# Kernel optimization log

Measured on AMD Instinct MI355X. Metric: run time of the kernel, lower is better.

Reference implementation:

```python
import jax, jax.numpy as jnp
import numpy as np

N, C, L, E, H = 2000, 4, 5000, 64000, 512
REP = 207  # length after conv front-end: floor((floor((5000-11)/4)+1 - 11)/6)+1


def setup_inputs() -> dict:
    key = jax.random.key(0)
    ks = jax.random.split(key, 10)

    def init(k, shape, fan_in):
        return jax.random.normal(k, shape, jnp.float32) / np.sqrt(fan_in).astype(np.float32)

    x = jax.random.normal(ks[0], (N, C, L), jnp.float32)
    edge_index = jax.random.randint(ks[1], (2, E), 0, N)
    return dict(
        x=x, edge_index=edge_index,
        w1=init(ks[2], (16, C, 1), C), b1=jnp.zeros(16, jnp.float32),
        w2=init(ks[3], (4, 4, 11), 4 * 11), b2=jnp.zeros(4, jnp.float32),
        w3=init(ks[4], (1, 4, 11), 4 * 11), b3=jnp.zeros(1, jnp.float32),
        gcn_w=init(ks[5], (REP, H), REP), gcn_b=jnp.zeros(H, jnp.float32),
        lin_w=init(ks[6], (REP, H), REP), lin_b=jnp.zeros(H, jnp.float32),
        gate_w=init(ks[7], (H, H), H), gate_b=jnp.zeros(H, jnp.float32),
        bn_gamma=jnp.ones(H, jnp.float32), bn_beta=jnp.zeros(H, jnp.float32),
    )


def _conv1d(x, w, b, stride):
    # x: [N, Cin, L], w: [Cout, Cin, K] (torch OIH layout), VALID padding
    y = jax.lax.conv_general_dilated(x, w, (stride,), 'VALID',
                                     dimension_numbers=('NCH', 'OIH', 'NCH'))
    return y + b[None, :, None]


def _gcn_conv(feat, edge_index, w, b, n):
    # GCNConv: x@W, add self-loops, sym-normalize, scatter-add, + bias
    h = feat @ w                                      # [N, H]
    loops = jnp.arange(n)
    src = jnp.concatenate([edge_index[0], loops])
    dst = jnp.concatenate([edge_index[1], loops])
    deg = jax.ops.segment_sum(jnp.ones_like(src, h.dtype), dst, num_segments=n)
    dinv = jax.lax.rsqrt(deg)                         # deg >= 1 due to self-loops
    norm = dinv[src] * dinv[dst]                      # [E+N]
    out = jax.ops.segment_sum(h[src] * norm[:, None], dst, num_segments=n)
    return out + b


def reference(x, edge_index, w1, b1, w2, b2, w3, b3,
              gcn_w, gcn_b, lin_w, lin_b, gate_w, gate_b, bn_gamma, bn_beta):
    n = x.shape[0]
    # conv front-end (dropout layers are identity at inference)
    h = jax.nn.relu(_conv1d(x, w1, b1, 1))            # [N, 16, L]
    # MaxPool1d(k=4,s=4) applied on permuted [N, L, 16] == pool over channel dim
    h = h.reshape(n, 4, 4, L).max(axis=2)             # [N, 4, L]
    h = jax.nn.relu(_conv1d(h, w2, b2, 4))            # [N, 4, 1248]
    h = jax.nn.relu(_conv1d(h, w3, b3, 6))            # [N, 1, 207]
    feat = h[:, 0, :]                                 # squeeze -> [N, REP]
    # GCN + gated fusion
    z = jnp.tanh(_gcn_conv(feat, edge_index, gcn_w, gcn_b, n))
    g = jax.nn.sigmoid(z @ gate_w + gate_b)
    xl = feat @ lin_w + lin_b
    out = jax.nn.relu((1.0 - g) * xl + g * z)
    # BatchNorm over node dim (batch statistics, training-mode semantics)
    mean = out.mean(axis=0)
    var = out.var(axis=0)
    out = (out - mean) * jax.lax.rsqrt(var + 1e-5) * bn_gamma + bn_beta
    return out
```

## Files before the change

### kernel.cpp

```cpp
#include <hip/hip_runtime.h>
#include <hip/hip_bf16.h>
#include <cstddef>

#define NN 2000
#define CC 4
#define LL1 5000
#define LL2 1248
#define LL3 207
#define FSTR 208
#define HH 512
#define EE 64000

__device__ float g_feat[NN * FSTR];
__device__ float g_aggf[NN * FSTR];
__device__ float g_z[NN * HH];
__device__ float g_xl[NN * HH];
__device__ float g_obuf[NN * HH];
__device__ float g_dinv[NN];
__device__ float g_colsum[HH];
__device__ float g_colsq[HH];
__device__ int   g_cnt[NN];
__device__ int   g_cursor[NN];
__device__ int   g_off[NN];
__device__ int   g_bucket[EE];

#define MCH 1256
__global__ __launch_bounds__(256) void conv_chain(
    const float* __restrict__ x, const int* __restrict__ ei, const int E,
    const float* __restrict__ w1, const float* __restrict__ b1,
    const float* __restrict__ w2, const float* __restrict__ b2,
    const float* __restrict__ w3, const float* __restrict__ b3)
{
    __shared__ __align__(16) float sm[4 * MCH];
    __shared__ __align__(16) float sy[4 * LL2];

    const int tid = threadIdx.x;
    const int node = blockIdx.x;

    if (node < 2) {
        int i = node * 256 + tid;
        g_colsum[i] = 0.f; g_colsq[i] = 0.f;
    }
    if (node < 250) {
        for (int e = node * 256 + tid; e < E; e += 250 * 256)
            atomicAdd(&g_cnt[ei[E + e]], 1);
    }

    const float* xb = x + (size_t)node * (CC * LL1);

    float w1r[64], b1r[16];
#pragma unroll
    for (int i = 0; i < 64; ++i) w1r[i] = w1[i];
#pragma unroll
    for (int i = 0; i < 16; ++i) b1r[i] = b1[i];

    float4 xA[2][4], xB[2][4];

    auto issueL = [&](int cc, float4 (&dst)[2][4]) {
#pragma unroll
        for (int it = 0; it < 2; ++it) {
            const int g4 = tid + it * 256;
            if (g4 < 314) {
                const int l = 1248 * cc + 4 * g4;
#pragma unroll
                for (int ch = 0; ch < 4; ++ch)
                    dst[it][ch] = *(const float4*)(xb + ch * LL1 + l);
            }
        }
    };

    auto stage1 = [&](float4 (&src)[2][4]) {
#pragma unroll
        for (int it = 0; it < 2; ++it) {
            const int g4 = tid + it * 256;
            if (g4 < 314) {
                float xs[4][4];
#pragma unroll
                for (int ch = 0; ch < 4; ++ch)
                    *(float4*)xs[ch] = src[it][ch];
#pragma unroll
                for (int g = 0; g < 4; ++g) {
                    float mv[4];
#pragma unroll
                    for (int li = 0; li < 4; ++li) {
                        float best = -1e30f;
#pragma unroll
                        for (int j = 0; j < 4; ++j) {
                            int o = g * 4 + j;
                            float v = b1r[o] + w1r[o*4+0]*xs[0][li] + w1r[o*4+1]*xs[1][li]
                                             + w1r[o*4+2]*xs[2][li] + w1r[o*4+3]*xs[3][li];
                            best = fmaxf(best, v);
                        }
                        mv[li] = fmaxf(best, 0.f);
                    }
                    *(float4*)&sm[g * MCH + 4 * g4] = make_float4(mv[0], mv[1], mv[2], mv[3]);
                }
            }
        }
    };

    auto stage2 = [&](int cc) {
        const int T0 = 312 * cc;
#pragma unroll 1
        for (int pair = 0; pair < 2; ++pair) {
            const float* wp = w2 + 88 * pair;
            float wo[88];
#pragma unroll
            for (int i = 0; i < 88; ++i) wo[i] = wp[i];
            const float bo0 = b2[2 * pair], bo1 = b2[2 * pair + 1];
            for (int T = tid; T < 312; T += 256) {
                float a0 = bo0, a1 = bo1;
#pragma unroll
                for (int i = 0; i < 4; ++i) {
                    const float* mp = sm + i * MCH + 4 * T;
                    float4 u0 = *(const float4*)mp;
                    float4 u1 = *(const float4*)(mp + 4);
                    float4 u2 = *(const float4*)(mp + 8);
                    float v[12] = {u0.x, u0.y, u0.z, u0.w,
                                   u1.x, u1.y, u1.z, u1.w,
                                   u2.x, u2.y, u2.z, u2.w};
#pragma unroll
                    for (int k = 0; k < 11; ++k) {
                        a0 += wo[i * 11 + k] * v[k];
                        a1 += wo[44 + i * 11 + k] * v[k];
                    }
                }
                sy[(2 * pair) * LL2 + T0 + T]     = fmaxf(a0, 0.f);
                sy[(2 * pair + 1) * LL2 + T0 + T] = fmaxf(a1, 0.f);
            }
        }
    };

    issueL(0, xA);
    issueL(1, xB);
    stage1(xA); __syncthreads(); stage2(0); __syncthreads();
    issueL(2, xA);
    stage1(xB); __syncthreads(); stage2(1); __syncthreads();
    issueL(3, xB);
    stage1(xA); __syncthreads(); stage2(2); __syncthreads();
    stage1(xB); __syncthreads(); stage2(3); __syncthreads();

    if (tid < FSTR) {
        float acc = 0.f;
        if (tid < LL3) {
            acc = b3[0];
#pragma unroll
            for (int i = 0; i < 4; ++i)
#pragma unroll
                for (int k = 0; k < 11; ++k)
                    acc += w3[i * 11 + k] * sy[i * LL2 + 6 * tid + k];
            acc = fmaxf(acc, 0.f);
        }
        g_feat[(size_t)node * FSTR + tid] = acc;
    }
}

__global__ __launch_bounds__(256) void scan_dinv() {
    const int tid = threadIdx.x;
    const int base = tid * 8;
    int c[8];
#pragma unroll
    for (int k = 0; k < 8; ++k) c[k] = (base + k < NN) ? g_cnt[base + k] : 0;
    int pre[8]; int s = 0;
#pragma unroll
    for (int k = 0; k < 8; ++k) { pre[k] = s; s += c[k]; }
    const int lane = tid & 63;
    int ws = s;
#pragma unroll
    for (int d = 1; d < 64; d <<= 1) {
        int t = __shfl_up(ws, d, 64);
        if (lane >= d) ws += t;
    }
    __shared__ int wsum[4];
    const int wid = tid >> 6;
    if (lane == 63) wsum[wid] = ws;
    __syncthreads();
    int woff = 0;
#pragma unroll
    for (int w = 0; w < 4; ++w) if (w < wid) woff += wsum[w];
    const int toff = woff + ws - s;
#pragma unroll
    for (int k = 0; k < 8; ++k) {
        const int i = base + k;
        if (i < NN) {
            g_off[i] = toff + pre[k];
            g_dinv[i] = rsqrtf(1.0f + (float)c[k]);
        }
    }
}

__global__ void bucket_fill(const int* __restrict__ ei, int E) {
    int e = blockIdx.x * 256 + threadIdx.x;
    if (e < E) {
        int d = ei[E + e];
        int p = atomicAdd(&g_cursor[d], 1);
        g_bucket[g_off[d] + p] = ei[e];
    }
}

__global__ __launch_bounds__(256) void agg_feat() {
    const int sub = threadIdx.x >> 6;
    const int lane = threadIdx.x & 63;
    const int d = blockIdx.x * 4 + sub;
    if (lane >= 52) return;
    const float di = g_dinv[d];
    const int nb = g_cnt[d];
    const int base = g_off[d];
    const size_t co = (size_t)lane * 4;
    float4 a = *(const float4*)(g_feat + (size_t)d * FSTR + co);
    float ax = a.x * di, ay = a.y * di, az = a.z * di, aw = a.w * di;
    int j = 0;
    for (; j + 1 < nb; j += 2) {
        int s0 = g_bucket[base + j];
        int s1 = g_bucket[base + j + 1];
        float w0 = g_dinv[s0], w1 = g_dinv[s1];
        float4 f0 = *(const float4*)(g_feat + (size_t)s0 * FSTR + co);
        float4 f1 = *(const float4*)(g_feat + (size_t)s1 * FSTR + co);
        ax += f0.x * w0 + f1.x * w1;
        ay += f0.y * w0 + f1.y * w1;
        az += f0.z * w0 + f1.z * w1;
        aw += f0.w * w0 + f1.w * w1;
    }
    if (j < nb) {
        int s = g_bucket[base + j];
        float w = g_dinv[s];
        float4 f = *(const float4*)(g_feat + (size_t)s * FSTR + co);
        ax += f.x * w; ay += f.y * w; az += f.z * w; aw += f.w * w;
    }
    *(float4*)(g_aggf + (size_t)d * FSTR + co) = make_float4(ax * di, ay * di, az * di, aw * di);
}

__global__ __launch_bounds__(256) void gemm_zxl(
    const float* __restrict__ gcn_w, const float* __restrict__ gcn_b,
    const float* __restrict__ lin_w, const float* __restrict__ lin_b)
{
    __shared__ __align__(16) float As[2][16][68];
    __shared__ __align__(16) float Bs[2][16][68];
    const int tid = threadIdx.x;
    const int which = blockIdx.z;
    const float* __restrict__ A = which ? g_feat : g_aggf;
    const float* __restrict__ B = which ? lin_w : gcn_w;
    const float* __restrict__ bias = which ? lin_b : gcn_b;
    float* __restrict__ C = which ? g_xl : g_z;
    const int N0 = blockIdx.x * 64, M0 = blockIdx.y * 64;
    const int ar = tid >> 2, ak = (tid & 3) * 4;
    const int bk = tid >> 4, bn = (tid & 15) * 4;
    const int ty = tid >> 4, tx = tid & 15;
    const int rowA = M0 + ar;

    float acc[16];
#pragma unroll
    for (int i = 0; i < 16; ++i) acc[i] = 0.f;
    const float4 z4 = make_float4(0.f, 0.f, 0.f, 0.f);
    float4 rA, rB;

    rA = (rowA < NN) ? *(const float4*)(A + (size_t)rowA * FSTR + ak) : z4;
    rB = (bk < LL3) ? *(const float4*)(B + (size_t)bk * HH + N0 + bn) : z4;
    As[0][ak+0][ar] = rA.x; As[0][ak+1][ar] = rA.y;
    As[0][ak+2][ar] = rA.z; As[0][ak+3][ar] = rA.w;
    *(float4*)&Bs[0][bk][bn] = rB;
    __syncthreads();

#pragma unroll 1
    for (int kt = 0; kt < 13; ++kt) {
        const int cur = kt & 1;
        if (kt + 1 < 13) {
            const int k0 = (kt + 1) * 16;
            rA = (rowA < NN) ? *(const float4*)(A + (size_t)rowA * FSTR + k0 + ak) : z4;
            const int kb = k0 + bk;
            rB = (kb < LL3) ? *(const float4*)(B + (size_t)kb * HH + N0 + bn) : z4;
        }
#pragma unroll
        for (int k = 0; k < 16; ++k) {
            const float4 a4 = *(const float4*)&As[cur][k][ty * 4];
            const float4 b4 = *(const float4*)&Bs[cur][k][tx * 4];
            const float av[4] = {a4.x, a4.y, a4.z, a4.w};
            const float bv[4] = {b4.x, b4.y, b4.z, b4.w};
#pragma unroll
            for (int i = 0; i < 4; ++i)
#pragma unroll
                for (int j = 0; j < 4; ++j)
                    acc[i * 4 + j] += av[i] * bv[j];
        }
        if (kt + 1 < 13) {
            const int nxt = cur ^ 1;
            As[nxt][ak+0][ar] = rA.x; As[nxt][ak+1][ar] = rA.y;
            As[nxt][ak+2][ar] = rA.z; As[nxt][ak+3][ar] = rA.w;
            *(float4*)&Bs[nxt][bk][bn] = rB;
        }
        __syncthreads();
    }

    const int c0 = N0 + tx * 4;
    const float4 bb = *(const float4*)(bias + c0);
#pragma unroll
    for (int i = 0; i < 4; ++i) {
        const int r = M0 + ty * 4 + i;
        if (r < NN) {
            float4 v = make_float4(acc[i*4+0] + bb.x, acc[i*4+1] + bb.y,
                                   acc[i*4+2] + bb.z, acc[i*4+3] + bb.w);
            if (which == 0) { v.x = tanhf(v.x); v.y = tanhf(v.y); v.z = tanhf(v.z); v.w = tanhf(v.w); }
            *(float4*)(C + (size_t)r * HH + c0) = v;
        }
    }
}

__global__ __launch_bounds__(256) void gemm_gate(
    const float* __restrict__ gate_w, const float* __restrict__ gate_b)
{
    __shared__ __align__(16) float As[2][16][68];
    __shared__ __align__(16) float Bs[2][16][68];
    __shared__ float rs[64], rq[64];
    const int tid = threadIdx.x;
    const float* __restrict__ A = g_z;
    const int N0 = blockIdx.x * 64, M0 = blockIdx.y * 64;
    const int ar = tid >> 2, ak = (tid & 3) * 4;
    const int bk = tid >> 4, bn = (tid & 15) * 4;
    const int ty = tid >> 4, tx = tid & 15;
    const int rowA = M0 + ar;

    float acc[16];
#pragma unroll
    for (int i = 0; i < 16; ++i) acc[i] = 0.f;
    const float4 z4 = make_float4(0.f, 0.f, 0.f, 0.f);
    float4 rA, rB;

    rA = (rowA < NN) ? *(const float4*)(A + (size_t)rowA * HH + ak) : z4;
    rB = *(const float4*)(gate_w + (size_t)bk * HH + N0 + bn);
    As[0][ak+0][ar] = rA.x; As[0][ak+1][ar] = rA.y;
    As[0][ak+2][ar] = rA.z; As[0][ak+3][ar] = rA.w;
    *(float4*)&Bs[0][bk][bn] = rB;
    __syncthreads();

#pragma unroll 1
    for (int kt = 0; kt < 32; ++kt) {
        const int cur = kt & 1;
        if (kt + 1 < 32) {
            const int k0 = (kt + 1) * 16;
            rA = (rowA < NN) ? *(const float4*)(A + (size_t)rowA * HH + k0 + ak) : z4;
            rB = *(const float4*)(gate_w + (size_t)(k0 + bk) * HH + N0 + bn);
        }
#pragma unroll
        for (int k = 0; k < 16; ++k) {
            const float4 a4 = *(const float4*)&As[cur][k][ty * 4];
            const float4 b4 = *(const float4*)&Bs[cur][k][tx * 4];
            const float av[4] = {a4.x, a4.y, a4.z, a4.w};
            const float bv[4] = {b4.x, b4.y, b4.z, b4.w};
#pragma unroll
            for (int i = 0; i < 4; ++i)
#pragma unroll
                for (int j = 0; j < 4; ++j)
                    acc[i * 4 + j] += av[i] * bv[j];
        }
        if (kt + 1 < 32) {
            const int nxt = cur ^ 1;
            As[nxt][ak+0][ar] = rA.x; As[nxt][ak+1][ar] = rA.y;
            As[nxt][ak+2][ar] = rA.z; As[nxt][ak+3][ar] = rA.w;
            *(float4*)&Bs[nxt][bk][bn] = rB;
        }
        __syncthreads();
    }

    const int c0 = N0 + tx * 4;
    const float4 bb = *(const float4*)(gate_b + c0);
    float cs[4] = {0.f, 0.f, 0.f, 0.f}, cq[4] = {0.f, 0.f, 0.f, 0.f};
#pragma unroll
    for (int i = 0; i < 4; ++i) {
        const int r = M0 + ty * 4 + i;
        if (r < NN) {
            const float4 xv = *(const float4*)(g_xl + (size_t)r * HH + c0);
            const float4 zv = *(const float4*)(g_z + (size_t)r * HH + c0);
            const float pre[4] = {acc[i*4+0] + bb.x, acc[i*4+1] + bb.y,
                                  acc[i*4+2] + bb.z, acc[i*4+3] + bb.w};
            const float xa[4] = {xv.x, xv.y, xv.z, xv.w};
            const float za[4] = {zv.x, zv.y, zv.z, zv.w};
            float va[4];
#pragma unroll
            for (int j = 0; j < 4; ++j) {
                float g = 1.f / (1.f + __expf(-pre[j]));
                float v = fmaxf((1.f - g) * xa[j] + g * za[j], 0.f);
                va[j] = v; cs[j] += v; cq[j] += v * v;
            }
            *(float4*)(g_obuf + (size_t)r * HH + c0) = make_float4(va[0], va[1], va[2], va[3]);
        }
    }
    if (tid < 64) { rs[tid] = 0.f; rq[tid] = 0.f; }
    __syncthreads();
#pragma unroll
    for (int j = 0; j < 4; ++j) {
        atomicAdd(&rs[tx * 4 + j], cs[j]);
        atomicAdd(&rq[tx * 4 + j], cq[j]);
    }
    __syncthreads();
    if (tid < 64) {
        atomicAdd(&g_colsum[N0 + tid], rs[tid]);
        atomicAdd(&g_colsq[N0 + tid], rq[tid]);
    }
}

__global__ __launch_bounds__(256) void bn_apply(const float* __restrict__ gamma,
                                                const float* __restrict__ beta,
                                                float* __restrict__ out) {
    if (blockIdx.x < 8) {
        int i = blockIdx.x * 256 + threadIdx.x;
        if (i < NN) { g_cnt[i] = 0; g_cursor[i] = 0; }
    }
    int i = blockIdx.x * 256 + threadIdx.x;
    int c = i & (HH - 1);
    float mean = g_colsum[c] * (1.f / (float)NN);
    float var = g_colsq[c] * (1.f / (float)NN) - mean * mean;
    float s = rsqrtf(var + 1e-5f) * gamma[c];
    out[i] = g_obuf[i] * s + (beta[c] - mean * s);
}

extern "C" void kernel_launch(void* const* d_in, const int* in_sizes, int n_in,
                              void* d_out, int out_size, void* d_ws, size_t ws_size,
                              hipStream_t stream) {
    (void)d_ws; (void)ws_size; (void)n_in; (void)out_size;
    const float* x      = (const float*)d_in[0];
    const int*   ei     = (const int*)d_in[1];
    const float* w1     = (const float*)d_in[2];
    const float* b1     = (const float*)d_in[3];
    const float* w2     = (const float*)d_in[4];
    const float* b2     = (const float*)d_in[5];
    const float* w3     = (const float*)d_in[6];
    const float* b3     = (const float*)d_in[7];
    const float* gcn_w  = (const float*)d_in[8];
    const float* gcn_b  = (const float*)d_in[9];
    const float* lin_w  = (const float*)d_in[10];
    const float* lin_b  = (const float*)d_in[11];
    const float* gate_w = (const float*)d_in[12];
    const float* gate_b = (const float*)d_in[13];
    const float* bn_g   = (const float*)d_in[14];
    const float* bn_b   = (const float*)d_in[15];
    float* out = (float*)d_out;
    const int E = in_sizes[1] / 2;

    conv_chain<<<NN, 256, 0, stream>>>(x, ei, E, w1, b1, w2, b2, w3, b3);
    scan_dinv<<<1, 256, 0, stream>>>();
    bucket_fill<<<(E + 255) / 256, 256, 0, stream>>>(ei, E);
    agg_feat<<<NN / 4, 256, 0, stream>>>();

    gemm_zxl<<<dim3(HH / 64, (NN + 63) / 64, 2), 256, 0, stream>>>(gcn_w, gcn_b, lin_w, lin_b);
    gemm_gate<<<dim3(HH / 64, (NN + 63) / 64), 256, 0, stream>>>(gate_w, gate_b);

    bn_apply<<<(NN * HH) / 256, 256, 0, stream>>>(bn_g, bn_b, out);
}
```

Before: 369.3 us.

## Stream conv3 per chunk with halo buffer to shrink conv2 shared buffer

Stage 3 (the final stride-6 conv) now runs per 312-column chunk instead of once at the end, so stage 2's output buffer shrinks from the full 1248 columns to a single chunk, with a small halo buffer carrying the 6 tail columns across chunks. The stage-3 work for a chunk is interleaved with stage 1 of the next chunk. This reduces LDS use, which could allow more resident blocks, and removes the serial tail at the end. In exchange it adds branchy halo indexing and more stage phases, with stage 3 running on only about 52 threads per chunk.

```diff
diff --git a/kernel.cpp b/kernel.cpp
--- a/kernel.cpp
+++ b/kernel.cpp
@@ -32,7 +32,8 @@
     const float* __restrict__ w3, const float* __restrict__ b3)
 {
     __shared__ __align__(16) float sm[4 * MCH];
-    __shared__ __align__(16) float sy[4 * LL2];
+    __shared__ __align__(16) float syc[4 * 312];
+    __shared__ float hb[2][4][6];
 
     const int tid = threadIdx.x;
     const int node = blockIdx.x;
@@ -100,7 +101,7 @@
     };
 
     auto stage2 = [&](int cc) {
-        const int T0 = 312 * cc;
+        (void)cc;
 #pragma unroll 1
         for (int pair = 0; pair < 2; ++pair) {
             const float* wp = w2 + 88 * pair;
@@ -125,34 +126,60 @@
                         a1 += wo[44 + i * 11 + k] * v[k];
                     }
                 }
-                sy[(2 * pair) * LL2 + T0 + T]     = fmaxf(a0, 0.f);
-                sy[(2 * pair + 1) * LL2 + T0 + T] = fmaxf(a1, 0.f);
+                syc[(2 * pair) * 312 + T]     = fmaxf(a0, 0.f);
+                syc[(2 * pair + 1) * 312 + T] = fmaxf(a1, 0.f);
             }
+        }
+    };
+
+    auto stage3 = [&](int cc) {
+        const int cnt = cc ? 52 : 51;
+        if (tid < cnt) {
+            const int t = cc ? (52 * cc - 1 + tid) : tid;
+            const int T0 = 312 * cc;
+            float acc = b3[0];
+#pragma unroll
+            for (int i = 0; i < 4; ++i)
+#pragma unroll
+                for (int k = 0; k < 11; ++k) {
+                    const int q = 6 * t + k - T0;
+                    const float v = (q < 0) ? hb[cc & 1][i][q + 6] : syc[i * 312 + q];
+                    acc += w3[i * 11 + k] * v;
+                }
+            g_feat[(size_t)node * FSTR + t] = fmaxf(acc, 0.f);
+        }
+    };
+
+    auto copyhead = [&](int cc) {
+        const int th = tid - 52;
+        if (th >= 0 && th < 24) {
+            const int ch = th / 6, j = th - 6 * ch;
+            hb[cc & 1][ch][j] = syc[ch * 312 + 306 + j];
         }
     };
 
     issueL(0, xA);
     issueL(1, xB);
-    stage1(xA); __syncthreads(); stage2(0); __syncthreads();
+    stage1(xA);
+    __syncthreads();
     issueL(2, xA);
-    stage1(xB); __syncthreads(); stage2(1); __syncthreads();
+    stage2(0);
+    __syncthreads();
+    stage1(xB); stage3(0); copyhead(1);
+    __syncthreads();
     issueL(3, xB);
-    stage1(xA); __syncthreads(); stage2(2); __syncthreads();
-    stage1(xB); __syncthreads(); stage2(3); __syncthreads();
-
-    if (tid < FSTR) {
-        float acc = 0.f;
-        if (tid < LL3) {
-            acc = b3[0];
-#pragma unroll
-            for (int i = 0; i < 4; ++i)
-#pragma unroll
-                for (int k = 0; k < 11; ++k)
-                    acc += w3[i * 11 + k] * sy[i * LL2 + 6 * tid + k];
-            acc = fmaxf(acc, 0.f);
-        }
-        g_feat[(size_t)node * FSTR + tid] = acc;
-    }
+    stage2(1);
+    __syncthreads();
+    stage1(xA); stage3(1); copyhead(2);
+    __syncthreads();
+    stage2(2);
+    __syncthreads();
+    stage1(xB); stage3(2); copyhead(3);
+    __syncthreads();
+    stage2(3);
+    __syncthreads();
+    stage3(3);
+    if (tid == 52) g_feat[(size_t)node * FSTR + 207] = 0.f;
 }
 
 __global__ __launch_bounds__(256) void scan_dinv() {
```

New measurement: 374.9 us. About the same (+1.5%).

## Split conv front-end into per-wavefront chunks to remove block barriers

Applied to the files above, without the earlier changes.

The conv_chain front-end is restructured so each wavefront independently processes overlapping 244-sample chunks (61 stage-2 outputs each) through a private shared-memory buffer. This removes the eight block-wide __syncthreads between stage1 and stage2, and replaces the per-pair register-cached w2 weights with direct loads computing all four output channels at once. Input loads are double-buffered per wavefront. The cost is redundant halo computation (about 4 of every 61 outputs' worth of inputs), a tail imbalance across 21 chunks for 4 wavefronts, and possible extra scalar loads of w2 inside the inner loop.

```diff
diff --git a/kernel.cpp b/kernel.cpp
--- a/kernel.cpp
+++ b/kernel.cpp
@@ -24,18 +24,19 @@
 __device__ int   g_off[NN];
 __device__ int   g_bucket[EE];
 
-#define MCH 1256
 __global__ __launch_bounds__(256) void conv_chain(
     const float* __restrict__ x, const int* __restrict__ ei, const int E,
     const float* __restrict__ w1, const float* __restrict__ b1,
     const float* __restrict__ w2, const float* __restrict__ b2,
     const float* __restrict__ w3, const float* __restrict__ b3)
 {
-    __shared__ __align__(16) float sm[4 * MCH];
-    __shared__ __align__(16) float sy[4 * LL2];
-
-    const int tid = threadIdx.x;
+    __shared__ __align__(16) float sy[4][LL2];
+    __shared__ __align__(16) float smw[4][4][256];
+
+    const int tid  = threadIdx.x;
     const int node = blockIdx.x;
+    const int wid  = tid >> 6;
+    const int lane = tid & 63;
 
     if (node < 2) {
         int i = node * 256 + tid;
@@ -54,65 +55,54 @@
 #pragma unroll
     for (int i = 0; i < 16; ++i) b1r[i] = b1[i];
 
-    float4 xA[2][4], xB[2][4];
-
-    auto issueL = [&](int cc, float4 (&dst)[2][4]) {
-#pragma unroll
-        for (int it = 0; it < 2; ++it) {
-            const int g4 = tid + it * 256;
-            if (g4 < 314) {
-                const int l = 1248 * cc + 4 * g4;
-#pragma unroll
-                for (int ch = 0; ch < 4; ++ch)
-                    dst[it][ch] = *(const float4*)(xb + ch * LL1 + l);
+    auto loadx = [&](int bb, float4 (&dst)[4]) {
+        const int p = 244 * bb + 4 * lane;
+        const bool ok = (p + 3) < LL1;
+#pragma unroll
+        for (int ch = 0; ch < 4; ++ch)
+            dst[ch] = ok ? *(const float4*)(xb + ch * LL1 + p)
+                         : make_float4(0.f, 0.f, 0.f, 0.f);
+    };
+
+    float4 xc[4], xn[4];
+    int b = wid;
+    if (b < 21) loadx(b, xc);
+
+    while (b < 21) {
+        const int bn = b + 4;
+        if (bn < 21) loadx(bn, xn);
+
+        {
+            float xs[4][4];
+#pragma unroll
+            for (int ch = 0; ch < 4; ++ch)
+                *(float4*)xs[ch] = xc[ch];
+#pragma unroll
+            for (int g = 0; g < 4; ++g) {
+                float mv[4];
+#pragma unroll
+                for (int li = 0; li < 4; ++li) {
+                    float best = -1e30f;
+#pragma unroll
+                    for (int j = 0; j < 4; ++j) {
+                        const int o = g * 4 + j;
+                        float v = b1r[o] + w1r[o*4+0]*xs[0][li] + w1r[o*4+1]*xs[1][li]
+                                         + w1r[o*4+2]*xs[2][li] + w1r[o*4+3]*xs[3][li];
+                        best = fmaxf(best, v);
+                    }
+                    mv[li] = fmaxf(best, 0.f);
+                }
+                *(float4*)&smw[wid][g][4 * lane] = make_float4(mv[0], mv[1], mv[2], mv[3]);
             }
         }
-    };
-
-    auto stage1 = [&](float4 (&src)[2][4]) {
-#pragma unroll
-        for (int it = 0; it < 2; ++it) {
-            const int g4 = tid + it * 256;
-            if (g4 < 314) {
-                float xs[4][4];
-#pragma unroll
-                for (int ch = 0; ch < 4; ++ch)
-                    *(float4*)xs[ch] = src[it][ch];
-#pragma unroll
-                for (int g = 0; g < 4; ++g) {
-                    float mv[4];
-#pragma unroll
-                    for (int li = 0; li < 4; ++li) {
-                        float best = -1e30f;
-#pragma unroll
-                        for (int j = 0; j < 4; ++j) {
-                            int o = g * 4 + j;
-                            float v = b1r[o] + w1r[o*4+0]*xs[0][li] + w1r[o*4+1]*xs[1][li]
-                                             + w1r[o*4+2]*xs[2][li] + w1r[o*4+3]*xs[3][li];
-                            best = fmaxf(best, v);
-                        }
-                        mv[li] = fmaxf(best, 0.f);
-                    }
-                    *(float4*)&sm[g * MCH + 4 * g4] = make_float4(mv[0], mv[1], mv[2], mv[3]);
-                }
-            }
-        }
-    };
-
-    auto stage2 = [&](int cc) {
-        const int T0 = 312 * cc;
-#pragma unroll 1
-        for (int pair = 0; pair < 2; ++pair) {
-            const float* wp = w2 + 88 * pair;
-            float wo[88];
-#pragma unroll
-            for (int i = 0; i < 88; ++i) wo[i] = wp[i];
-            const float bo0 = b2[2 * pair], bo1 = b2[2 * pair + 1];
-            for (int T = tid; T < 312; T += 256) {
-                float a0 = bo0, a1 = bo1;
+
+        {
+            const int Tg = 61 * b + lane;
+            if (lane < 61 && Tg < LL2) {
+                float a0 = b2[0], a1 = b2[1], a2 = b2[2], a3 = b2[3];
 #pragma unroll
                 for (int i = 0; i < 4; ++i) {
-                    const float* mp = sm + i * MCH + 4 * T;
+                    const float* mp = &smw[wid][i][4 * lane];
                     float4 u0 = *(const float4*)mp;
                     float4 u1 = *(const float4*)(mp + 4);
                     float4 u2 = *(const float4*)(mp + 8);
@@ -121,24 +111,25 @@
                                    u2.x, u2.y, u2.z, u2.w};
 #pragma unroll
                     for (int k = 0; k < 11; ++k) {
-                        a0 += wo[i * 11 + k] * v[k];
-                        a1 += wo[44 + i * 11 + k] * v[k];
+                        a0 += w2[  0 + i * 11 + k] * v[k];
+                        a1 += w2[ 44 + i * 11 + k] * v[k];
+                        a2 += w2[ 88 + i * 11 + k] * v[k];
+                        a3 += w2[132 + i * 11 + k] * v[k];
                     }
                 }
-                sy[(2 * pair) * LL2 + T0 + T]     = fmaxf(a0, 0.f);
-                sy[(2 * pair + 1) * LL2 + T0 + T] = fmaxf(a1, 0.f);
+                sy[0][Tg] = fmaxf(a0, 0.f);
+                sy[1][Tg] = fmaxf(a1, 0.f);
+                sy[2][Tg] = fmaxf(a2, 0.f);
+                sy[3][Tg] = fmaxf(a3, 0.f);
             }
         }
-    };
-
-    issueL(0, xA);
-    issueL(1, xB);
-    stage1(xA); __syncthreads(); stage2(0); __syncthreads();
-    issueL(2, xA);
-    stage1(xB); __syncthreads(); stage2(1); __syncthreads();
-    issueL(3, xB);
-    stage1(xA); __syncthreads(); stage2(2); __syncthreads();
-    stage1(xB); __syncthreads(); stage2(3); __syncthreads();
+
+#pragma unroll
+        for (int ch = 0; ch < 4; ++ch) xc[ch] = xn[ch];
+        b = bn;
+    }
+
+    __syncthreads();
 
     if (tid < FSTR) {
         float acc = 0.f;
@@ -148,7 +139,7 @@
             for (int i = 0; i < 4; ++i)
 #pragma unroll
                 for (int k = 0; k < 11; ++k)
-                    acc += w3[i * 11 + k] * sy[i * LL2 + 6 * tid + k];
+                    acc += w3[i * 11 + k] * sy[i][6 * tid + k];
             acc = fmaxf(acc, 0.f);
         }
         g_feat[(size_t)node * FSTR + tid] = acc;
```

Result: no change. 365.7 us (-1.0%).
